# Performance work log

Hardware: AMD Instinct MI355X
Metric: run time of the kernel (lower is better)

## Reference

```python
import jax, jax.numpy as jnp
import numpy as np

N, E, G = 50000, 1600000, 512
IN_DIM, HEADS, C1, C2, HIDDEN = 128, 3, 32, 32, 512
NEG_SLOPE = 0.2
EPS = 1e-16


def _glorot(key, shape):
    fan_in = shape[0]
    return jax.random.normal(key, shape, dtype=jnp.float32) / np.sqrt(fan_in)


def setup_inputs() -> dict:
    key = jax.random.key(0)
    ks = jax.random.split(key, 16)
    x = jax.random.normal(ks[0], (N, IN_DIM), dtype=jnp.float32)
    edge_index = jax.random.randint(ks[1], (2, E), 0, N, dtype=jnp.int64)
    batch = (jnp.arange(N, dtype=jnp.int64) * G) // N  # sorted, all graphs non-empty
    d1, d2 = HEADS * C1, HEADS * C2
    return {
        "x": x,
        "W_l1": _glorot(ks[2], (IN_DIM, d1)), "b_l1": jnp.zeros((d1,), jnp.float32),
        "W_r1": _glorot(ks[3], (IN_DIM, d1)), "b_r1": jnp.zeros((d1,), jnp.float32),
        "att1": _glorot(ks[4], (HEADS, C1)), "bias1": jnp.zeros((d1,), jnp.float32),
        "W_l2": _glorot(ks[5], (d1, d2)), "b_l2": jnp.zeros((d2,), jnp.float32),
        "W_r2": _glorot(ks[6], (d1, d2)), "b_r2": jnp.zeros((d2,), jnp.float32),
        "att2": _glorot(ks[7], (HEADS, C2)), "bias2": jnp.zeros((d2,), jnp.float32),
        "W_fc1": _glorot(ks[8], (d1 + d2, HIDDEN)), "b_fc1": jnp.zeros((HIDDEN,), jnp.float32),
        "W_fc2": _glorot(ks[9], (HIDDEN, 2)), "b_fc2": jnp.zeros((2,), jnp.float32),
        "edge_index": edge_index,
        "batch": batch,
    }


def gatv2_conv(xin, src, dst, W_l, b_l, W_r, b_r, att, bias, heads, out_c):
    n = xin.shape[0]
    x_l = (xin @ W_l + b_l).reshape(n, heads, out_c)  # source-side projection
    x_r = (xin @ W_r + b_r).reshape(n, heads, out_c)  # target-side projection
    e = jax.nn.leaky_relu(x_l[src] + x_r[dst], NEG_SLOPE)  # [E', H, C]
    logits = jnp.einsum("ehc,hc->eh", e, att)  # [E', H]
    m = jax.ops.segment_max(logits, dst, num_segments=n)
    a = jnp.exp(logits - m[dst])
    denom = jax.ops.segment_sum(a, dst, num_segments=n)
    alpha = a / (denom[dst] + EPS)  # per-destination edge softmax (PyG semantics)
    out = jax.ops.segment_sum(x_l[src] * alpha[:, :, None], dst, num_segments=n)
    return out.reshape(n, heads * out_c) + bias


def reference(x, W_l1, b_l1, W_r1, b_r1, att1, bias1,
              W_l2, b_l2, W_r2, b_r2, att2, bias2,
              W_fc1, b_fc1, W_fc2, b_fc2, edge_index, batch):
    n = x.shape[0]
    loop = jnp.arange(n, dtype=edge_index.dtype)
    src = jnp.concatenate([edge_index[0], loop])  # PyG GATv2Conv adds self-loops
    dst = jnp.concatenate([edge_index[1], loop])
    h1 = jnp.tanh(gatv2_conv(x, src, dst, W_l1, b_l1, W_r1, b_r1, att1, bias1, HEADS, C1))
    h2 = jnp.tanh(gatv2_conv(h1, src, dst, W_l2, b_l2, W_r2, b_r2, att2, bias2, HEADS, C2))
    h = jnp.concatenate([h1, h2], axis=1)  # [N, (C1+C2)*H]
    first_idx = jnp.searchsorted(batch, jnp.arange(G, dtype=batch.dtype))  # first node of each graph
    pooled = h[first_idx]  # [G, (C1+C2)*H]
    hidden = jax.nn.relu(pooled @ W_fc1 + b_fc1)
    logits = hidden @ W_fc2 + b_fc2
    return jax.nn.log_softmax(logits, axis=1)
```

## Files before the change

kernel.cpp:

```cpp
#include <hip/hip_runtime.h>
#include <hip/hip_bf16.h>
#include <hip/hip_fp16.h>
#include <math.h>

#define NN 50000
#define EE 1600000
#define GG 512
#define INDIM 128
#define HEADS 3
#define CC 32
#define DD 96
#define HID 512
#define NEG 0.2f
#define EPS_DEN 1e-16f
#define CAP 128
#define MNEG -1e30f

#define OFF_WL1   0
#define OFF_BL1   12288
#define OFF_WR1   12384
#define OFF_BR1   24672
#define OFF_ATT1  24768
#define OFF_BIAS1 24864
#define OFF_WL2   24960
#define OFF_BL2   34176
#define OFF_WR2   34272
#define OFF_BR2   43488
#define OFF_ATT2  43584
#define OFF_BIAS2 43680
#define OFF_WFC1  43776
#define OFF_BFC1  142080
#define OFF_WFC2  142592
#define OFF_BFC2  143616
#define P_TOTAL   143744

typedef _Float16 h8 __attribute__((ext_vector_type(8)));
typedef float f4 __attribute__((ext_vector_type(4)));

static __device__ __forceinline__ float bf2f(__hip_bfloat16 v) { return __bfloat162float(v); }

static __device__ __forceinline__ int getI(const void* p, long long i, bool w64) {
    return w64 ? ((const int*)p)[2 * i] : ((const int*)p)[i];
}

static __device__ __forceinline__ void load4(const void* p, int base, int e0, bool w64, int* v) {
    const int4* q = (const int4*)p;
    if (w64) {
        int4 a = q[(base + e0) >> 1];
        int4 b = q[((base + e0) >> 1) + 1];
        v[0] = a.x; v[1] = a.z; v[2] = b.x; v[3] = b.z;
    } else {
        int4 a = q[(base + e0) >> 2];
        v[0] = a.x; v[1] = a.y; v[2] = a.z; v[3] = a.w;
    }
}

__global__ void detect_kernel(const void* __restrict__ x, const void* __restrict__ ei,
                              int* __restrict__ flags)
{
    __shared__ int wild, zcnt;
    if (threadIdx.x == 0) { wild = 0; zcnt = 0; }
    __syncthreads();
    int w = 0, z = 0;
    const __hip_bfloat16* xb = (const __hip_bfloat16*)x;
    for (int i = threadIdx.x; i < 4096; i += 256) {
        float v = bf2f(xb[i]);
        if (!(fabsf(v) <= 1e6f)) w++;
    }
    const int* e32 = (const int*)ei;
    for (int i = threadIdx.x; i < 4096; i += 256) {
        if (e32[2 * i + 1] == 0) z++;
    }
    atomicAdd(&wild, w);
    atomicAdd(&zcnt, z);
    __syncthreads();
    if (threadIdx.x == 0) {
        flags[0] = (wild < 64) ? 1 : 0;
        flags[1] = (zcnt > 4000) ? 1 : 0;
    }
}

struct ParamTab { const void* p[16]; int sz[16]; int off[16]; };

__global__ void convert_params_kernel(ParamTab t, const int* __restrict__ flags,
                                      float* __restrict__ P)
{
    const int which = blockIdx.y;
    const int n = t.sz[which];
    const void* src = t.p[which];
    float* dst = P + t.off[which];
    const bool isbf = flags[0] != 0;
    for (int i = blockIdx.x * 256 + threadIdx.x; i < n; i += gridDim.x * 256) {
        dst[i] = isbf ? bf2f(((const __hip_bfloat16*)src)[i]) : ((const float*)src)[i];
    }
}

__global__ void build_bswz_kernel(const float* __restrict__ P, int offWl, int offWr, int KC,
                                  __half* __restrict__ B)
{
    int idx = blockIdx.x * 256 + threadIdx.x;
    int total = 12 * KC * 64;
    if (idx >= total) return;
    int lane = idx & 63;
    int t = idx >> 6;
    int kc = t % KC;
    int ntile = t / KC;
    int n = ntile * 16 + (lane & 15);
    int kbase = kc * 32 + (lane >> 4) * 8;
    const float* Wsrc = (n < 96) ? (P + offWl) : (P + offWr);
    int n2 = (n < 96) ? n : n - 96;
    __half* dst = B + (size_t)idx * 8;
#pragma unroll
    for (int j = 0; j < 8; j++) dst[j] = __float2half(Wsrc[(kbase + j) * 96 + n2]);
}

__global__ void firstpool_kernel(const void* __restrict__ batch, const int* __restrict__ flags,
                                 int* __restrict__ first, int* __restrict__ pooled,
                                 int* __restrict__ needed)
{
    int i = blockIdx.x * 256 + threadIdx.x;
    if (i >= NN) return;
    const bool w64 = flags[1] != 0;
    int b = getI(batch, i, w64);
    if (i == 0 || getI(batch, i - 1, w64) != b) {
        first[b] = i;
        pooled[i] = 1;
        needed[i] = 1;
    }
}

__global__ void mark_needed_kernel(const void* __restrict__ ei, const int* __restrict__ flags,
                                   const int* __restrict__ pooled, int* __restrict__ needed)
{
    int e0 = (blockIdx.x * 256 + threadIdx.x) * 4;
    if (e0 >= EE) return;
    const bool w64 = flags[1] != 0;
    int s4[4], d4[4];
    load4(ei, EE, e0, w64, d4);
    load4(ei, 0, e0, w64, s4);
#pragma unroll
    for (int j = 0; j < 4; j++) if (pooled[d4[j]]) needed[s4[j]] = 1;
}

__global__ void compact_kernel(const int* __restrict__ needed, int* __restrict__ list,
                               int* __restrict__ cnt)
{
    int i = blockIdx.x * 256 + threadIdx.x;
    if (i >= NN) return;
    if (needed[i]) list[atomicAdd(cnt, 1)] = i;
}

__global__ void scatter_fixed_kernel(const void* __restrict__ ei, const int* __restrict__ flags,
                                     const int* __restrict__ needed,
                                     int* __restrict__ deg, int* __restrict__ csr)
{
    int e0 = (blockIdx.x * 256 + threadIdx.x) * 4;
    if (e0 >= EE) return;
    const bool w64 = flags[1] != 0;
    int s4[4], d4[4];
    load4(ei, EE, e0, w64, d4);
    load4(ei, 0, e0, w64, s4);
#pragma unroll
    for (int j = 0; j < 4; j++) {
        int dst = d4[j];
        if (!needed[dst]) continue;
        int pos = atomicAdd(&deg[dst], 1);
        if (pos < CAP) csr[(size_t)dst * CAP + pos] = s4[j];
    }
}

template <int KDIM, int MODE>
__global__ __launch_bounds__(256) void proj_mfma_kernel(
    const void* __restrict__ Ain, const __half* __restrict__ Bswz,
    const int* __restrict__ list, const int* __restrict__ cnt,
    const float* __restrict__ P, const int* __restrict__ flags, int offBl, int offBr,
    __half* __restrict__ xl, float* __restrict__ xr)
{
    constexpr int KC = KDIM / 32;
    __shared__ __half Bs[12 * KC * 64 * 8];
    const int tid = threadIdx.x;
    const int limit = MODE ? *cnt : NN;
    const int blockBase = blockIdx.x * 64;
    if (blockBase >= limit) return;

    {
        const int chunks = 12 * KC * 64;
        for (int i = tid; i < chunks; i += 256)
            reinterpret_cast<f4*>(Bs)[i] = reinterpret_cast<const f4*>(Bswz)[i];
    }
    __syncthreads();

    const int wave = tid >> 6;
    const int lane = tid & 63;
    const int base = blockBase + wave * 16;
    if (base >= limit) return;

    const int q = lane >> 4;
    const int mlane = lane & 15;

    int aIdx = base + mlane;
    int aRow;
    if (MODE) aRow = (aIdx < limit) ? list[aIdx] : list[limit - 1];
    else      aRow = (aIdx < limit) ? aIdx : 0;

    h8 a[KC];
    if (MODE == 1) {
        const h8* arow = reinterpret_cast<const h8*>((const __half*)Ain + (size_t)aRow * KDIM);
#pragma unroll
        for (int kc = 0; kc < KC; kc++) a[kc] = arow[kc * 4 + q];
    } else if (flags[0]) {
        const int4* arow = reinterpret_cast<const int4*>((const ushort*)Ain + (size_t)aRow * KDIM);
#pragma unroll
        for (int kc = 0; kc < KC; kc++) {
            int4 r = arow[kc * 4 + q];
            int ws[4] = {r.x, r.y, r.z, r.w};
#pragma unroll
            for (int i = 0; i < 4; i++) {
                a[kc][2 * i]     = (_Float16)__int_as_float(ws[i] << 16);
                a[kc][2 * i + 1] = (_Float16)__int_as_float(ws[i] & 0xffff0000);
            }
        }
    } else {
        const f4* arow = reinterpret_cast<const f4*>((const float*)Ain + (size_t)aRow * KDIM);
#pragma unroll
        for (int kc = 0; kc < KC; kc++) {
            f4 r0 = arow[kc * 8 + q * 2];
            f4 r1 = arow[kc * 8 + q * 2 + 1];
#pragma unroll
            for (int i = 0; i < 4; i++) {
                a[kc][i]     = (_Float16)r0[i];
                a[kc][4 + i] = (_Float16)r1[i];
            }
        }
    }

    int sRow[4];
#pragma unroll
    for (int r = 0; r < 4; r++) {
        int si = base + q * 4 + r;
        sRow[r] = (si < limit) ? (MODE ? list[si] : si) : -1;
    }

    const h8* Bf = reinterpret_cast<const h8*>(Bs);
#pragma unroll
    for (int ntile = 0; ntile < 12; ntile++) {
        int n = ntile * 16 + mlane;
        float bv = (n < 96) ? P[offBl + n] : P[offBr + n - 96];
        f4 acc = {bv, bv, bv, bv};
#pragma unroll
        for (int kc = 0; kc < KC; kc++) {
            h8 b = Bf[(ntile * KC + kc) * 64 + lane];
            acc = __builtin_amdgcn_mfma_f32_16x16x32_f16(a[kc], b, acc, 0, 0, 0);
        }
#pragma unroll
        for (int r = 0; r < 4; r++) {
            if (sRow[r] < 0) continue;
            if (n < 96) xl[(size_t)sRow[r] * DD + n] = __float2half(acc[r]);
            else        xr[(size_t)sRow[r] * DD + (n - 96)] = acc[r];
        }
    }
}

template <int OUTMODE>
__global__ __launch_bounds__(256) void fused_edge_kernel(
    const int* __restrict__ csr, const int* __restrict__ deg,
    const int* __restrict__ list, const int* __restrict__ cnt,
    const __half* __restrict__ xl, const float* __restrict__ xr,
    const float* __restrict__ P, int offAtt, int offBias,
    void* __restrict__ out)
{
    const int lane = threadIdx.x & 63;
    const int c = lane & 31;
    const int eo = lane >> 5;
    const int w0 = (blockIdx.x * 256 + threadIdx.x) >> 6;
    const int nw = (gridDim.x * 256) >> 6;
    const int limit = (OUTMODE == 0) ? *cnt : GG;
    const int items = limit * 3;

    for (int item = w0; item < items; item += nw) {
        const int li = item / 3;
        const int h = item - li * 3;
        const int n = list[li];
        const int hc = h * CC + c;

        const float attc = P[offAtt + hc];
        const float xr_c = xr[(size_t)n * DD + hc];

        float m, d, o;
        {
            float xls = __half2float(xl[(size_t)n * DD + hc]);
            float s = xls + xr_c;
            s = s > 0.0f ? s : NEG * s;
            float p = s * attc;
#pragma unroll
            for (int off = 16; off; off >>= 1) p += __shfl_xor(p, off, 32);
            if (eo == 0) { m = p; d = 1.0f; o = xls; }
            else         { m = MNEG; d = 0.0f; o = 0.0f; }
        }

        const int* row = csr + (size_t)n * CAP;
        const int end = min(deg[n], CAP);
        int k = eo;
        for (; k + 6 < end; k += 8) {
            int s0 = row[k], s1 = row[k + 2], s2 = row[k + 4], s3 = row[k + 6];
            float x0 = __half2float(xl[(size_t)s0 * DD + hc]);
            float x1 = __half2float(xl[(size_t)s1 * DD + hc]);
            float x2 = __half2float(xl[(size_t)s2 * DD + hc]);
            float x3 = __half2float(xl[(size_t)s3 * DD + hc]);
            float t0 = x0 + xr_c; t0 = t0 > 0.0f ? t0 : NEG * t0;
            float t1 = x1 + xr_c; t1 = t1 > 0.0f ? t1 : NEG * t1;
            float t2 = x2 + xr_c; t2 = t2 > 0.0f ? t2 : NEG * t2;
            float t3 = x3 + xr_c; t3 = t3 > 0.0f ? t3 : NEG * t3;
            float q0 = t0 * attc, q1 = t1 * attc, q2 = t2 * attc, q3 = t3 * attc;
#pragma unroll
            for (int off = 16; off; off >>= 1) {
                q0 += __shfl_xor(q0, off, 32);
                q1 += __shfl_xor(q1, off, 32);
                q2 += __shfl_xor(q2, off, 32);
                q3 += __shfl_xor(q3, off, 32);
            }
            if (q0 <= m) { float e = __expf(q0 - m); d += e; o += e * x0; }
            else         { float r2 = __expf(m - q0); d = d * r2 + 1.0f; o = o * r2 + x0; m = q0; }
            if (q1 <= m) { float e = __expf(q1 - m); d += e; o += e * x1; }
            else         { float r2 = __expf(m - q1); d = d * r2 + 1.0f; o = o * r2 + x1; m = q1; }
            if (q2 <= m) { float e = __expf(q2 - m); d += e; o += e * x2; }
            else         { float r2 = __expf(m - q2); d = d * r2 + 1.0f; o = o * r2 + x2; m = q2; }
            if (q3 <= m) { float e = __expf(q3 - m); d += e; o += e * x3; }
            else         { float r2 = __expf(m - q3); d = d * r2 + 1.0f; o = o * r2 + x3; m = q3; }
        }
        for (; k < end; k += 2) {
            int src = row[k];
            float xv = __half2float(xl[(size_t)src * DD + hc]);
            float s = xv + xr_c;
            s = s > 0.0f ? s : NEG * s;
            float p = s * attc;
#pragma unroll
            for (int off = 16; off; off >>= 1) p += __shfl_xor(p, off, 32);
            if (p <= m) { float e = __expf(p - m); d += e; o += e * xv; }
            else        { float r2 = __expf(m - p); d = d * r2 + 1.0f; o = o * r2 + xv; m = p; }
        }

        float m2 = __shfl_xor(m, 32);
        float d2 = __shfl_xor(d, 32);
        float o2 = __shfl_xor(o, 32);
        float nm = fmaxf(m, m2);
        float e1 = __expf(m - nm), e2 = __expf(m2 - nm);
        d = d * e1 + d2 * e2;
        o = o * e1 + o2 * e2;

        float res = tanhf(o / (d + EPS_DEN) + P[offBias + hc]);
        if (eo == 0) {
            if (OUTMODE == 0) ((__half*)out)[(size_t)n * DD + hc] = __float2half(res);
            else              ((float*)out)[(size_t)li * DD + hc] = res;
        }
    }
}

__global__ __launch_bounds__(256) void mlp_kernel(
    const __half* __restrict__ h1h, const float* __restrict__ h2p,
    const float* __restrict__ P, const int* __restrict__ flags,
    const int* __restrict__ first, void* __restrict__ outv)
{
    __shared__ float pooled[2 * DD];
    __shared__ float hidden[HID];
    __shared__ float r0[4], r1[4];
    const int g = blockIdx.x;
    const int t = threadIdx.x;
    const int row = first[g];

    if (t < DD) pooled[t] = __half2float(h1h[(size_t)row * DD + t]);
    else if (t < 2 * DD) pooled[t] = h2p[(size_t)g * DD + (t - DD)];
    __syncthreads();

    for (int col = t; col < HID; col += 256) {
        float acc = P[OFF_BFC1 + col];
        for (int i = 0; i < 2 * DD; i++) acc += pooled[i] * P[OFF_WFC1 + i * HID + col];
        hidden[col] = fmaxf(acc, 0.0f);
    }
    __syncthreads();

    float p0 = 0.0f, p1 = 0.0f;
    for (int j = t; j < HID; j += 256) {
        float hv = hidden[j];
        p0 += hv * P[OFF_WFC2 + j * 2 + 0];
        p1 += hv * P[OFF_WFC2 + j * 2 + 1];
    }
#pragma unroll
    for (int off = 32; off > 0; off >>= 1) {
        p0 += __shfl_down(p0, off);
        p1 += __shfl_down(p1, off);
    }
    int w = t >> 6;
    if ((t & 63) == 0) { r0[w] = p0; r1[w] = p1; }
    __syncthreads();
    if (t == 0) {
        float l0 = r0[0] + r0[1] + r0[2] + r0[3] + P[OFF_BFC2 + 0];
        float l1 = r1[0] + r1[1] + r1[2] + r1[3] + P[OFF_BFC2 + 1];
        float mx = fmaxf(l0, l1);
        float lse = mx + logf(expf(l0 - mx) + expf(l1 - mx));
        float o0 = l0 - lse, o1 = l1 - lse;
        if (flags[0]) {
            ((__hip_bfloat16*)outv)[g * 2 + 0] = __float2bfloat16(o0);
            ((__hip_bfloat16*)outv)[g * 2 + 1] = __float2bfloat16(o1);
        } else {
            ((float*)outv)[g * 2 + 0] = o0;
            ((float*)outv)[g * 2 + 1] = o1;
        }
    }
}

extern "C" void kernel_launch(void* const* d_in, const int* in_sizes, int n_in,
                              void* d_out, int out_size, void* d_ws, size_t ws_size,
                              hipStream_t stream)
{
    const void* x     = d_in[0];
    const void* ei    = d_in[17];
    const void* batch = d_in[18];

    float* ws   = (float*)d_ws;
    float* P    = ws;
    float* xr   = P + P_TOTAL;
    float* h2p  = xr + (size_t)NN * DD;

    __half* hp   = (__half*)(h2p + (size_t)GG * DD);
    __half* xlh  = hp;
    __half* xl2h = xlh + (size_t)NN * DD;
    __half* h1h  = xl2h + (size_t)NN * DD;
    __half* B1   = h1h + (size_t)NN * DD;
    __half* B2   = B1 + 24576;

    int* ip      = (int*)(B2 + 18432);
    int* deg     = ip;
    int* pooled  = deg + NN;
    int* needed  = pooled + NN;
    int* cnt     = needed + NN;
    int* csr     = cnt + 4;
    int* list    = csr + (size_t)NN * CAP;
    int* first   = list + NN;
    int* flags   = first + GG;

    ParamTab t;
    const int sz[16]  = {12288, 96, 12288, 96, 96, 96, 9216, 96, 9216, 96, 96, 96, 98304, 512, 1024, 2};
    const int off[16] = {OFF_WL1, OFF_BL1, OFF_WR1, OFF_BR1, OFF_ATT1, OFF_BIAS1,
                         OFF_WL2, OFF_BL2, OFF_WR2, OFF_BR2, OFF_ATT2, OFF_BIAS2,
                         OFF_WFC1, OFF_BFC1, OFF_WFC2, OFF_BFC2};
    for (int i = 0; i < 16; i++) { t.p[i] = d_in[1 + i]; t.sz[i] = sz[i]; t.off[i] = off[i]; }

    const int edge4B = (EE / 4 + 255) / 256;
    const int nodeB = (NN + 255) / 256;
    const int mprojB = (NN + 63) / 64;
    const int fuse1B = 2048;
    const int fuse2B = (GG * 3) / 4;

    detect_kernel<<<1, 256, 0, stream>>>(x, ei, flags);
    convert_params_kernel<<<dim3(96, 16), 256, 0, stream>>>(t, flags, P);
    build_bswz_kernel<<<12, 256, 0, stream>>>(P, OFF_WL1, OFF_WR1, 4, B1);
    build_bswz_kernel<<<9, 256, 0, stream>>>(P, OFF_WL2, OFF_WR2, 3, B2);
    (void)hipMemsetAsync(deg, 0, (size_t)(3 * NN + 4) * sizeof(int), stream);

    firstpool_kernel<<<nodeB, 256, 0, stream>>>(batch, flags, first, pooled, needed);
    mark_needed_kernel<<<edge4B, 256, 0, stream>>>(ei, flags, pooled, needed);
    compact_kernel<<<nodeB, 256, 0, stream>>>(needed, list, cnt);

    scatter_fixed_kernel<<<edge4B, 256, 0, stream>>>(ei, flags, needed, deg, csr);

    proj_mfma_kernel<INDIM, 0><<<mprojB, 256, 0, stream>>>(x, B1, nullptr, nullptr,
                                                           P, flags, OFF_BL1, OFF_BR1, xlh, xr);
    fused_edge_kernel<0><<<fuse1B, 256, 0, stream>>>(csr, deg, list, cnt, xlh, xr,
                                                     P, OFF_ATT1, OFF_BIAS1, (void*)h1h);

    proj_mfma_kernel<DD, 1><<<mprojB, 256, 0, stream>>>(h1h, B2, list, cnt,
                                                        P, flags, OFF_BL2, OFF_BR2, xl2h, xr);
    fused_edge_kernel<1><<<fuse2B, 256, 0, stream>>>(csr, deg, first, nullptr, xl2h, xr,
                                                     P, OFF_ATT2, OFF_BIAS2, (void*)h2p);

    mlp_kernel<<<GG, 256, 0, stream>>>(h1h, h2p, P, flags, first, d_out);
}
```

Measured before the change: 280.9 us.

## Use bitmaps for node marks, MFMA MLP head, and cheaper leaky-relu

Replaces the int-per-node pooled/needed arrays with packed bitmaps set by atomicOr, which shrinks the memset and the gathered footprint in the edge-scan kernels. The per-graph scalar MLP is replaced by an fp16 MFMA kernel that fuses fc1, relu, fc2 and log_softmax, using a pre-swizzled fc1 weight buffer and a gathered A matrix. The leaky-relu becomes fmin+fma and the index arithmetic drops the 64-bit multiply. In exchange it adds atomics on shared bitmap words and two extra small kernels, and the fc1 matmul now runs in fp16.

```diff
diff --git a/kernel.cpp b/kernel.cpp
--- a/kernel.cpp
+++ b/kernel.cpp
@@ -12,9 +12,11 @@
 #define DD 96
 #define HID 512
 #define NEG 0.2f
+#define NEGM1 (NEG - 1.0f)
 #define EPS_DEN 1e-16f
 #define CAP 128
 #define MNEG -1e30f
+#define NBW 1568
 
 #define OFF_WL1   0
 #define OFF_BL1   12288
@@ -55,6 +57,10 @@
     }
 }
 
+static __device__ __forceinline__ bool testbit(const unsigned* b, int i) {
+    return (b[i >> 5] >> (i & 31)) & 1u;
+}
+
 __global__ void detect_kernel(const void* __restrict__ x, const void* __restrict__ ei,
                               int* __restrict__ flags)
 {
@@ -114,9 +120,26 @@
     for (int j = 0; j < 8; j++) dst[j] = __float2half(Wsrc[(kbase + j) * 96 + n2]);
 }
 
+__global__ void build_bswz_fc_kernel(const float* __restrict__ P, __half* __restrict__ B)
+{
+    int idx = blockIdx.x * 256 + threadIdx.x;
+    const int total = 32 * 6 * 64;
+    if (idx >= total) return;
+    int lane = idx & 63;
+    int t = idx >> 6;
+    int kc = t % 6;
+    int ntile = t / 6;
+    int n = ntile * 16 + (lane & 15);
+    int kbase = kc * 32 + (lane >> 4) * 8;
+    const float* W = P + OFF_WFC1;
+    __half* dst = B + (size_t)idx * 8;
+#pragma unroll
+    for (int j = 0; j < 8; j++) dst[j] = __float2half(W[(kbase + j) * HID + n]);
+}
+
 __global__ void firstpool_kernel(const void* __restrict__ batch, const int* __restrict__ flags,
-                                 int* __restrict__ first, int* __restrict__ pooled,
-                                 int* __restrict__ needed)
+                                 int* __restrict__ first, unsigned* __restrict__ pb,
+                                 unsigned* __restrict__ nb)
 {
     int i = blockIdx.x * 256 + threadIdx.x;
     if (i >= NN) return;
@@ -124,13 +147,13 @@
     int b = getI(batch, i, w64);
     if (i == 0 || getI(batch, i - 1, w64) != b) {
         first[b] = i;
-        pooled[i] = 1;
-        needed[i] = 1;
+        atomicOr(&pb[i >> 5], 1u << (i & 31));
+        atomicOr(&nb[i >> 5], 1u << (i & 31));
     }
 }
 
 __global__ void mark_needed_kernel(const void* __restrict__ ei, const int* __restrict__ flags,
-                                   const int* __restrict__ pooled, int* __restrict__ needed)
+                                   const unsigned* __restrict__ pb, unsigned* __restrict__ nb)
 {
     int e0 = (blockIdx.x * 256 + threadIdx.x) * 4;
     if (e0 >= EE) return;
@@ -139,19 +162,20 @@
     load4(ei, EE, e0, w64, d4);
     load4(ei, 0, e0, w64, s4);
 #pragma unroll
-    for (int j = 0; j < 4; j++) if (pooled[d4[j]]) needed[s4[j]] = 1;
-}
-
-__global__ void compact_kernel(const int* __restrict__ needed, int* __restrict__ list,
+    for (int j = 0; j < 4; j++)
+        if (testbit(pb, d4[j])) atomicOr(&nb[s4[j] >> 5], 1u << (s4[j] & 31));
+}
+
+__global__ void compact_kernel(const unsigned* __restrict__ nb, int* __restrict__ list,
                                int* __restrict__ cnt)
 {
     int i = blockIdx.x * 256 + threadIdx.x;
     if (i >= NN) return;
-    if (needed[i]) list[atomicAdd(cnt, 1)] = i;
+    if (testbit(nb, i)) list[atomicAdd(cnt, 1)] = i;
 }
 
 __global__ void scatter_fixed_kernel(const void* __restrict__ ei, const int* __restrict__ flags,
-                                     const int* __restrict__ needed,
+                                     const unsigned* __restrict__ nb,
                                      int* __restrict__ deg, int* __restrict__ csr)
 {
     int e0 = (blockIdx.x * 256 + threadIdx.x) * 4;
@@ -163,7 +187,7 @@
 #pragma unroll
     for (int j = 0; j < 4; j++) {
         int dst = d4[j];
-        if (!needed[dst]) continue;
+        if (!testbit(nb, dst)) continue;
         int pos = atomicAdd(&deg[dst], 1);
         if (pos < CAP) csr[(size_t)dst * CAP + pos] = s4[j];
     }
@@ -267,7 +291,7 @@
     const int* __restrict__ list, const int* __restrict__ cnt,
     const __half* __restrict__ xl, const float* __restrict__ xr,
     const float* __restrict__ P, int offAtt, int offBias,
-    void* __restrict__ out)
+    __half* __restrict__ out)
 {
     const int lane = threadIdx.x & 63;
     const int c = lane & 31;
@@ -282,15 +306,16 @@
         const int h = item - li * 3;
         const int n = list[li];
         const int hc = h * CC + c;
+        const __half* xlb = xl + hc;
 
         const float attc = P[offAtt + hc];
         const float xr_c = xr[(size_t)n * DD + hc];
 
         float m, d, o;
         {
-            float xls = __half2float(xl[(size_t)n * DD + hc]);
+            float xls = __half2float(xlb[n * DD]);
             float s = xls + xr_c;
-            s = s > 0.0f ? s : NEG * s;
+            s = fmaf(fminf(s, 0.0f), NEGM1, s);
             float p = s * attc;
 #pragma unroll
             for (int off = 16; off; off >>= 1) p += __shfl_xor(p, off, 32);
@@ -303,14 +328,14 @@
         int k = eo;
         for (; k + 6 < end; k += 8) {
             int s0 = row[k], s1 = row[k + 2], s2 = row[k + 4], s3 = row[k + 6];
-            float x0 = __half2float(xl[(size_t)s0 * DD + hc]);
-            float x1 = __half2float(xl[(size_t)s1 * DD + hc]);
-            float x2 = __half2float(xl[(size_t)s2 * DD + hc]);
-            float x3 = __half2float(xl[(size_t)s3 * DD + hc]);
-            float t0 = x0 + xr_c; t0 = t0 > 0.0f ? t0 : NEG * t0;
-            float t1 = x1 + xr_c; t1 = t1 > 0.0f ? t1 : NEG * t1;
-            float t2 = x2 + xr_c; t2 = t2 > 0.0f ? t2 : NEG * t2;
-            float t3 = x3 + xr_c; t3 = t3 > 0.0f ? t3 : NEG * t3;
+            float x0 = __half2float(xlb[s0 * DD]);
+            float x1 = __half2float(xlb[s1 * DD]);
+            float x2 = __half2float(xlb[s2 * DD]);
+            float x3 = __half2float(xlb[s3 * DD]);
+            float t0 = x0 + xr_c; t0 = fmaf(fminf(t0, 0.0f), NEGM1, t0);
+            float t1 = x1 + xr_c; t1 = fmaf(fminf(t1, 0.0f), NEGM1, t1);
+            float t2 = x2 + xr_c; t2 = fmaf(fminf(t2, 0.0f), NEGM1, t2);
+            float t3 = x3 + xr_c; t3 = fmaf(fminf(t3, 0.0f), NEGM1, t3);
             float q0 = t0 * attc, q1 = t1 * attc, q2 = t2 * attc, q3 = t3 * attc;
 #pragma unroll
             for (int off = 16; off; off >>= 1) {
@@ -330,9 +355,9 @@
         }
         for (; k < end; k += 2) {
             int src = row[k];
-            float xv = __half2float(xl[(size_t)src * DD + hc]);
+            float xv = __half2float(xlb[src * DD]);
             float s = xv + xr_c;
-            s = s > 0.0f ? s : NEG * s;
+            s = fmaf(fminf(s, 0.0f), NEGM1, s);
             float p = s * attc;
 #pragma unroll
             for (int off = 16; off; off >>= 1) p += __shfl_xor(p, off, 32);
@@ -350,61 +375,76 @@
 
         float res = tanhf(o / (d + EPS_DEN) + P[offBias + hc]);
         if (eo == 0) {
-            if (OUTMODE == 0) ((__half*)out)[(size_t)n * DD + hc] = __float2half(res);
-            else              ((float*)out)[(size_t)li * DD + hc] = res;
-        }
-    }
-}
-
-__global__ __launch_bounds__(256) void mlp_kernel(
-    const __half* __restrict__ h1h, const float* __restrict__ h2p,
-    const float* __restrict__ P, const int* __restrict__ flags,
-    const int* __restrict__ first, void* __restrict__ outv)
-{
-    __shared__ float pooled[2 * DD];
-    __shared__ float hidden[HID];
-    __shared__ float r0[4], r1[4];
-    const int g = blockIdx.x;
-    const int t = threadIdx.x;
-    const int row = first[g];
-
-    if (t < DD) pooled[t] = __half2float(h1h[(size_t)row * DD + t]);
-    else if (t < 2 * DD) pooled[t] = h2p[(size_t)g * DD + (t - DD)];
-    __syncthreads();
-
-    for (int col = t; col < HID; col += 256) {
-        float acc = P[OFF_BFC1 + col];
-        for (int i = 0; i < 2 * DD; i++) acc += pooled[i] * P[OFF_WFC1 + i * HID + col];
-        hidden[col] = fmaxf(acc, 0.0f);
-    }
-    __syncthreads();
-
-    float p0 = 0.0f, p1 = 0.0f;
-    for (int j = t; j < HID; j += 256) {
-        float hv = hidden[j];
-        p0 += hv * P[OFF_WFC2 + j * 2 + 0];
-        p1 += hv * P[OFF_WFC2 + j * 2 + 1];
-    }
-#pragma unroll
-    for (int off = 32; off > 0; off >>= 1) {
-        p0 += __shfl_down(p0, off);
-        p1 += __shfl_down(p1, off);
-    }
-    int w = t >> 6;
-    if ((t & 63) == 0) { r0[w] = p0; r1[w] = p1; }
-    __syncthreads();
-    if (t == 0) {
-        float l0 = r0[0] + r0[1] + r0[2] + r0[3] + P[OFF_BFC2 + 0];
-        float l1 = r1[0] + r1[1] + r1[2] + r1[3] + P[OFF_BFC2 + 1];
-        float mx = fmaxf(l0, l1);
-        float lse = mx + logf(expf(l0 - mx) + expf(l1 - mx));
-        float o0 = l0 - lse, o1 = l1 - lse;
-        if (flags[0]) {
-            ((__hip_bfloat16*)outv)[g * 2 + 0] = __float2bfloat16(o0);
-            ((__hip_bfloat16*)outv)[g * 2 + 1] = __float2bfloat16(o1);
-        } else {
-            ((float*)outv)[g * 2 + 0] = o0;
-            ((float*)outv)[g * 2 + 1] = o1;
+            if (OUTMODE == 0) out[(size_t)n * DD + hc] = __float2half(res);
+            else              out[(size_t)li * 192 + 96 + hc] = __float2half(res);
+        }
+    }
+}
+
+__global__ void gatherA_kernel(const __half* __restrict__ h1h, const int* __restrict__ first,
+                               __half* __restrict__ A)
+{
+    int idx = blockIdx.x * 256 + threadIdx.x;
+    if (idx >= GG * DD) return;
+    int g = idx / DD, c = idx - g * DD;
+    A[(size_t)g * 192 + c] = h1h[(size_t)first[g] * DD + c];
+}
+
+__global__ __launch_bounds__(256) void mlp_mfma_kernel(
+    const __half* __restrict__ A, const __half* __restrict__ Bfc,
+    const float* __restrict__ P, const int* __restrict__ flags, void* __restrict__ outv)
+{
+    const int tid = threadIdx.x;
+    const int wave = tid >> 6, lane = tid & 63;
+    const int q = lane >> 4, ml = lane & 15;
+    const int rowbase = blockIdx.x * 64 + wave * 16;
+
+    h8 a[6];
+    const h8* arow = reinterpret_cast<const h8*>(A + (size_t)(rowbase + ml) * 192);
+#pragma unroll
+    for (int kc = 0; kc < 6; kc++) a[kc] = arow[kc * 4 + q];
+
+    const h8* Bf = reinterpret_cast<const h8*>(Bfc);
+    const float* w2 = P + OFF_WFC2;
+    float p0[4] = {0, 0, 0, 0}, p1[4] = {0, 0, 0, 0};
+    for (int nt = 0; nt < 32; nt++) {
+        int n = nt * 16 + ml;
+        float bv = P[OFF_BFC1 + n];
+        f4 acc = {bv, bv, bv, bv};
+#pragma unroll
+        for (int kc = 0; kc < 6; kc++)
+            acc = __builtin_amdgcn_mfma_f32_16x16x32_f16(a[kc], Bf[(nt * 6 + kc) * 64 + lane], acc, 0, 0, 0);
+        float w20 = w2[2 * n], w21 = w2[2 * n + 1];
+#pragma unroll
+        for (int r = 0; r < 4; r++) {
+            float hdn = fmaxf(acc[r], 0.0f);
+            p0[r] = fmaf(hdn, w20, p0[r]);
+            p1[r] = fmaf(hdn, w21, p1[r]);
+        }
+    }
+#pragma unroll
+    for (int off = 1; off <= 8; off <<= 1) {
+#pragma unroll
+        for (int r = 0; r < 4; r++) {
+            p0[r] += __shfl_xor(p0[r], off);
+            p1[r] += __shfl_xor(p1[r], off);
+        }
+    }
+    if (ml == 0) {
+        float b0 = P[OFF_BFC2], b1 = P[OFF_BFC2 + 1];
+#pragma unroll
+        for (int r = 0; r < 4; r++) {
+            int g = rowbase + q * 4 + r;
+            float l0 = p0[r] + b0, l1 = p1[r] + b1;
+            float mx = fmaxf(l0, l1);
+            float lse = mx + logf(__expf(l0 - mx) + __expf(l1 - mx));
+            if (flags[0]) {
+                ((__hip_bfloat16*)outv)[g * 2 + 0] = __float2bfloat16(l0 - lse);
+                ((__hip_bfloat16*)outv)[g * 2 + 1] = __float2bfloat16(l1 - lse);
+            } else {
+                ((float*)outv)[g * 2 + 0] = l0 - lse;
+                ((float*)outv)[g * 2 + 1] = l1 - lse;
+            }
         }
     }
 }
@@ -420,24 +460,25 @@
     float* ws   = (float*)d_ws;
     float* P    = ws;
     float* xr   = P + P_TOTAL;
-    float* h2p  = xr + (size_t)NN * DD;
-
-    __half* hp   = (__half*)(h2p + (size_t)GG * DD);
+
+    __half* hp   = (__half*)(xr + (size_t)NN * DD);
     __half* xlh  = hp;
     __half* xl2h = xlh + (size_t)NN * DD;
     __half* h1h  = xl2h + (size_t)NN * DD;
-    __half* B1   = h1h + (size_t)NN * DD;
+    __half* A    = h1h + (size_t)NN * DD;
+    __half* B1   = A + (size_t)GG * 192;
     __half* B2   = B1 + 24576;
-
-    int* ip      = (int*)(B2 + 18432);
-    int* deg     = ip;
-    int* pooled  = deg + NN;
-    int* needed  = pooled + NN;
-    int* cnt     = needed + NN;
-    int* csr     = cnt + 4;
-    int* list    = csr + (size_t)NN * CAP;
-    int* first   = list + NN;
-    int* flags   = first + GG;
+    __half* Bfc  = B2 + 18432;
+
+    int* ip       = (int*)(Bfc + 98304);
+    int* deg      = ip;
+    unsigned* pb  = (unsigned*)(deg + NN);
+    unsigned* nb  = pb + NBW;
+    int* cnt      = (int*)(nb + NBW);
+    int* csr      = cnt + 4;
+    int* list     = csr + (size_t)NN * CAP;
+    int* first    = list + NN;
+    int* flags    = first + GG;
 
     ParamTab t;
     const int sz[16]  = {12288, 96, 12288, 96, 96, 96, 9216, 96, 9216, 96, 96, 96, 98304, 512, 1024, 2};
@@ -456,23 +497,25 @@
     convert_params_kernel<<<dim3(96, 16), 256, 0, stream>>>(t, flags, P);
     build_bswz_kernel<<<12, 256, 0, stream>>>(P, OFF_WL1, OFF_WR1, 4, B1);
     build_bswz_kernel<<<9, 256, 0, stream>>>(P, OFF_WL2, OFF_WR2, 3, B2);
-    (void)hipMemsetAsync(deg, 0, (size_t)(3 * NN + 4) * sizeof(int), stream);
-
-    firstpool_kernel<<<nodeB, 256, 0, stream>>>(batch, flags, first, pooled, needed);
-    mark_needed_kernel<<<edge4B, 256, 0, stream>>>(ei, flags, pooled, needed);
-    compact_kernel<<<nodeB, 256, 0, stream>>>(needed, list, cnt);
-
-    scatter_fixed_kernel<<<edge4B, 256, 0, stream>>>(ei, flags, needed, deg, csr);
+    build_bswz_fc_kernel<<<48, 256, 0, stream>>>(P, Bfc);
+    (void)hipMemsetAsync(deg, 0, (size_t)(NN + 2 * NBW + 4) * sizeof(int), stream);
+
+    firstpool_kernel<<<nodeB, 256, 0, stream>>>(batch, flags, first, pb, nb);
+    mark_needed_kernel<<<edge4B, 256, 0, stream>>>(ei, flags, pb, nb);
+    compact_kernel<<<nodeB, 256, 0, stream>>>(nb, list, cnt);
+
+    scatter_fixed_kernel<<<edge4B, 256, 0, stream>>>(ei, flags, nb, deg, csr);
 
     proj_mfma_kernel<INDIM, 0><<<mprojB, 256, 0, stream>>>(x, B1, nullptr, nullptr,
                                                            P, flags, OFF_BL1, OFF_BR1, xlh, xr);
     fused_edge_kernel<0><<<fuse1B, 256, 0, stream>>>(csr, deg, list, cnt, xlh, xr,
-                                                     P, OFF_ATT1, OFF_BIAS1, (void*)h1h);
+                                                     P, OFF_ATT1, OFF_BIAS1, h1h);
 
     proj_mfma_kernel<DD, 1><<<mprojB, 256, 0, stream>>>(h1h, B2, list, cnt,
                                                         P, flags, OFF_BL2, OFF_BR2, xl2h, xr);
     fused_edge_kernel<1><<<fuse2B, 256, 0, stream>>>(csr, deg, first, nullptr, xl2h, xr,
-                                                     P, OFF_ATT2, OFF_BIAS2, (void*)h2p);
-
-    mlp_kernel<<<GG, 256, 0, stream>>>(h1h, h2p, P, flags, first, d_out);
-}
+                                                     P, OFF_ATT2, OFF_BIAS2, A);
+
+    gatherA_kernel<<<(GG * DD + 255) / 256, 256, 0, stream>>>(h1h, first, A);
+    mlp_mfma_kernel<<<GG / 64, 256, 0, stream>>>(A, Bfc, P, flags, d_out);
+}
```

Result: slower. 297.5 us (+5.9%).
